# Performance work log

Hardware: AMD Instinct MI355X
Metric: run time of the kernel (lower is better)

## Reference

```python
import jax, jax.numpy as jnp
import numpy as np


def setup_inputs() -> dict:
    key = jax.random.key(0)
    x = jax.random.uniform(key, (64_000_000,), dtype=jnp.float32)
    return {"x": x, "bins": 100}


def reference(x, bins):
    # torch.histc semantics with min=max=0.0: use data min/max as the range.
    xf = x.reshape(-1)
    hmin = jnp.min(xf)
    hmax = jnp.max(xf)
    # guard degenerate range (torch widens it; with random data this is a no-op)
    hmax = jnp.where(hmax == hmin, hmin + 1.0, hmax)
    scale = bins / (hmax - hmin)
    # bin index: floor((x - min) * bins / (max - min)); value == max lands in last bin
    idx = jnp.clip(jnp.floor((xf - hmin) * scale).astype(jnp.int32), 0, bins - 1)
    in_range = (xf >= hmin) & (xf <= hmax)  # out-of-range elements are ignored
    weights = in_range.astype(xf.dtype)
    hist = jax.ops.segment_sum(weights, idx, num_segments=bins)
    return hist
```

## Files before the change

### kernel.cpp

```cpp
#include <hip/hip_runtime.h>

#define NBLOCKS   1024
#define NTHREADS  256
#define UNROLL_A  16
#define UNROLL_B  8
#define NCOPIES   32
#define CSTRIDE   101

__global__ __launch_bounds__(NTHREADS, 4)
void minmax_partial(const float4* __restrict__ x4, long n4,
                    const float* __restrict__ xtail, long ntail,
                    float* __restrict__ pmin, float* __restrict__ pmax,
                    float* __restrict__ out, int bins) {
    __shared__ float smin[NTHREADS / 64], smax[NTHREADS / 64];
    if (blockIdx.x == 0) {
        for (int b = threadIdx.x; b < bins; b += blockDim.x) out[b] = 0.0f;
    }
    const long tid = blockIdx.x * (long)blockDim.x + threadIdx.x;
    const long nth = (long)gridDim.x * blockDim.x;

    float m0 = INFINITY, M0 = -INFINITY, m1 = INFINITY, M1 = -INFINITY;
    float m2 = INFINITY, M2 = -INFINITY, m3 = INFINITY, M3 = -INFINITY;

    const long chunk   = nth * UNROLL_A;
    const long nchunks = n4 / chunk;

    for (long j = nchunks * chunk + tid; j < n4; j += nth) {
        float4 v = x4[j];
        m0 = fminf(m0, fminf(fminf(v.x, v.y), fminf(v.z, v.w)));
        M0 = fmaxf(M0, fmaxf(fmaxf(v.x, v.y), fmaxf(v.z, v.w)));
    }
    for (long j = tid; j < ntail; j += nth) {
        float v = xtail[j];
        m0 = fminf(m0, v);
        M0 = fmaxf(M0, v);
    }
    for (long c = nchunks; c-- > 0;) {
        const long j = c * chunk + tid;
        float4 v[UNROLL_A];
        #pragma unroll
        for (int u = 0; u < UNROLL_A; ++u) v[u] = x4[j + (long)u * nth];
        #pragma unroll
        for (int u = 0; u < UNROLL_A; u += 4) {
            m0 = fminf(m0, fminf(fminf(v[u].x, v[u].y), fminf(v[u].z, v[u].w)));
            M0 = fmaxf(M0, fmaxf(fmaxf(v[u].x, v[u].y), fmaxf(v[u].z, v[u].w)));
            m1 = fminf(m1, fminf(fminf(v[u+1].x, v[u+1].y), fminf(v[u+1].z, v[u+1].w)));
            M1 = fmaxf(M1, fmaxf(fmaxf(v[u+1].x, v[u+1].y), fmaxf(v[u+1].z, v[u+1].w)));
            m2 = fminf(m2, fminf(fminf(v[u+2].x, v[u+2].y), fminf(v[u+2].z, v[u+2].w)));
            M2 = fmaxf(M2, fmaxf(fmaxf(v[u+2].x, v[u+2].y), fmaxf(v[u+2].z, v[u+2].w)));
            m3 = fminf(m3, fminf(fminf(v[u+3].x, v[u+3].y), fminf(v[u+3].z, v[u+3].w)));
            M3 = fmaxf(M3, fmaxf(fmaxf(v[u+3].x, v[u+3].y), fmaxf(v[u+3].z, v[u+3].w)));
        }
    }

    float lm = fminf(fminf(m0, m1), fminf(m2, m3));
    float lM = fmaxf(fmaxf(M0, M1), fmaxf(M2, M3));
    for (int off = 32; off; off >>= 1) {
        lm = fminf(lm, __shfl_xor(lm, off));
        lM = fmaxf(lM, __shfl_xor(lM, off));
    }
    if ((threadIdx.x & 63) == 0) {
        smin[threadIdx.x >> 6] = lm;
        smax[threadIdx.x >> 6] = lM;
    }
    __syncthreads();
    if (threadIdx.x == 0) {
        float bm = smin[0], bM = smax[0];
        for (int w = 1; w < NTHREADS / 64; ++w) { bm = fminf(bm, smin[w]); bM = fmaxf(bM, smax[w]); }
        pmin[blockIdx.x] = bm;
        pmax[blockIdx.x] = bM;
    }
}

__global__ __launch_bounds__(NTHREADS, 4)
void hist_kernel(const float4* __restrict__ x4, long n4,
                 const float* __restrict__ xtail, long ntail,
                 const float* __restrict__ pmin, const float* __restrict__ pmax,
                 float* __restrict__ out, int bins) {
    __shared__ unsigned sh[NCOPIES * CSTRIDE];
    __shared__ float smin[NTHREADS / 64], smax[NTHREADS / 64];
    __shared__ float srange[2];

    float rm = INFINITY, rM = -INFINITY;
    for (int i = threadIdx.x; i < NBLOCKS; i += blockDim.x) {
        rm = fminf(rm, pmin[i]);
        rM = fmaxf(rM, pmax[i]);
    }
    for (int off = 32; off; off >>= 1) {
        rm = fminf(rm, __shfl_xor(rm, off));
        rM = fmaxf(rM, __shfl_xor(rM, off));
    }
    if ((threadIdx.x & 63) == 0) {
        smin[threadIdx.x >> 6] = rm;
        smax[threadIdx.x >> 6] = rM;
    }
    __syncthreads();
    if (threadIdx.x == 0) {
        float bm = smin[0], bM = smax[0];
        for (int w = 1; w < NTHREADS / 64; ++w) { bm = fminf(bm, smin[w]); bM = fmaxf(bM, smax[w]); }
        if (bM == bm) bM = bm + 1.0f;
        srange[0] = bm;
        srange[1] = (float)bins / (bM - bm);
    }
    for (int b = threadIdx.x; b < NCOPIES * CSTRIDE; b += blockDim.x) sh[b] = 0u;
    __syncthreads();

    const float hmin  = srange[0];
    const float scale = srange[1];
    const int   bmax  = bins - 1;
    unsigned* h = sh + (threadIdx.x >> 3) * CSTRIDE;

    const long tid = blockIdx.x * (long)blockDim.x + threadIdx.x;
    const long nth = (long)gridDim.x * blockDim.x;
    const long chunk   = nth * UNROLL_B;
    const long nchunks = n4 / chunk;

    for (long c = 0; c < nchunks; ++c) {
        const long j = c * chunk + tid;
        float4 v[UNROLL_B];
        #pragma unroll
        for (int u = 0; u < UNROLL_B; ++u) v[u] = x4[j + (long)u * nth];
        #pragma unroll
        for (int u = 0; u < UNROLL_B; ++u) {
            int b0 = min(max((int)((v[u].x - hmin) * scale), 0), bmax);
            int b1 = min(max((int)((v[u].y - hmin) * scale), 0), bmax);
            int b2 = min(max((int)((v[u].z - hmin) * scale), 0), bmax);
            int b3 = min(max((int)((v[u].w - hmin) * scale), 0), bmax);
            atomicAdd(&h[b0], 1u);
            atomicAdd(&h[b1], 1u);
            atomicAdd(&h[b2], 1u);
            atomicAdd(&h[b3], 1u);
        }
    }
    for (long j = nchunks * chunk + tid; j < n4; j += nth) {
        float4 v = x4[j];
        int b0 = min(max((int)((v.x - hmin) * scale), 0), bmax);
        int b1 = min(max((int)((v.y - hmin) * scale), 0), bmax);
        int b2 = min(max((int)((v.z - hmin) * scale), 0), bmax);
        int b3 = min(max((int)((v.w - hmin) * scale), 0), bmax);
        atomicAdd(&h[b0], 1u);
        atomicAdd(&h[b1], 1u);
        atomicAdd(&h[b2], 1u);
        atomicAdd(&h[b3], 1u);
    }
    for (long j = tid; j < ntail; j += nth) {
        int b0 = min(max((int)((xtail[j] - hmin) * scale), 0), bmax);
        atomicAdd(&h[b0], 1u);
    }
    __syncthreads();

    for (int b = threadIdx.x; b < bins; b += blockDim.x) {
        unsigned t = 0;
        #pragma unroll
        for (int w = 0; w < NCOPIES; ++w) t += sh[w * CSTRIDE + b];
        if (t) atomicAdd(&out[b], (float)t);
    }
}

extern "C" void kernel_launch(void* const* d_in, const int* in_sizes, int n_in,
                              void* d_out, int out_size, void* d_ws, size_t ws_size,
                              hipStream_t stream) {
    const float* x = (const float*)d_in[0];
    long n = (long)in_sizes[0];
    int bins = out_size;

    long n4 = n >> 2;
    long ntail = n - (n4 << 2);
    const float4* x4 = (const float4*)x;
    const float* xtail = x + (n4 << 2);

    float* out = (float*)d_out;
    float* ws = (float*)d_ws;
    float* pmin = ws;
    float* pmax = ws + NBLOCKS;

    minmax_partial<<<NBLOCKS, NTHREADS, 0, stream>>>(x4, n4, xtail, ntail,
                                                     pmin, pmax, out, bins);
    hist_kernel<<<NBLOCKS, NTHREADS, 0, stream>>>(x4, n4, xtail, ntail,
                                                  pmin, pmax, out, bins);
}
```

Before: 398.5 us.

## Use per-wave contiguous segments and per-lane LDS histogram copies

Both kernels now give each wavefront a contiguous segment of 64*UNROLL float4s in a grid-stride loop over segments, instead of a thread-strided chunked layout. The min/max pass walks segments in reverse order so the histogram pass, which walks them forward, may hit data still in cache. The histogram now keeps 64 LDS copies, one per lane, with stride 101 to cut atomic contention and bank conflicts, and the lower clamp at zero is dropped. The extra copies double LDS use and may lower occupancy. Removing the zero clamp assumes every value is at least the computed minimum.

```diff
diff --git a/kernel.cpp b/kernel.cpp
--- a/kernel.cpp
+++ b/kernel.cpp
@@ -2,9 +2,10 @@
 
 #define NBLOCKS   1024
 #define NTHREADS  256
+#define WPB       (NTHREADS / 64)
 #define UNROLL_A  16
 #define UNROLL_B  8
-#define NCOPIES   32
+#define NCOPIES   64
 #define CSTRIDE   101
 
 __global__ __launch_bounds__(NTHREADS, 4)
@@ -12,34 +13,39 @@
                     const float* __restrict__ xtail, long ntail,
                     float* __restrict__ pmin, float* __restrict__ pmax,
                     float* __restrict__ out, int bins) {
-    __shared__ float smin[NTHREADS / 64], smax[NTHREADS / 64];
+    __shared__ float smin[WPB], smax[WPB];
     if (blockIdx.x == 0) {
         for (int b = threadIdx.x; b < bins; b += blockDim.x) out[b] = 0.0f;
     }
-    const long tid = blockIdx.x * (long)blockDim.x + threadIdx.x;
-    const long nth = (long)gridDim.x * blockDim.x;
+    const int  lane   = threadIdx.x & 63;
+    const long gwave  = blockIdx.x * (long)WPB + (threadIdx.x >> 6);
+    const long nwaves = (long)gridDim.x * WPB;
+    const long SEG    = 64 * UNROLL_A;
+    const long nseg   = n4 / SEG;
 
     float m0 = INFINITY, M0 = -INFINITY, m1 = INFINITY, M1 = -INFINITY;
     float m2 = INFINITY, M2 = -INFINITY, m3 = INFINITY, M3 = -INFINITY;
 
-    const long chunk   = nth * UNROLL_A;
-    const long nchunks = n4 / chunk;
+    {
+        const long tid = blockIdx.x * (long)blockDim.x + threadIdx.x;
+        const long nth = (long)gridDim.x * blockDim.x;
+        for (long j = nseg * SEG + tid; j < n4; j += nth) {
+            float4 v = x4[j];
+            m0 = fminf(m0, fminf(fminf(v.x, v.y), fminf(v.z, v.w)));
+            M0 = fmaxf(M0, fmaxf(fmaxf(v.x, v.y), fmaxf(v.z, v.w)));
+        }
+        for (long j = tid; j < ntail; j += nth) {
+            float v = xtail[j];
+            m0 = fminf(m0, v);
+            M0 = fmaxf(M0, v);
+        }
+    }
 
-    for (long j = nchunks * chunk + tid; j < n4; j += nth) {
-        float4 v = x4[j];
-        m0 = fminf(m0, fminf(fminf(v.x, v.y), fminf(v.z, v.w)));
-        M0 = fmaxf(M0, fmaxf(fmaxf(v.x, v.y), fmaxf(v.z, v.w)));
-    }
-    for (long j = tid; j < ntail; j += nth) {
-        float v = xtail[j];
-        m0 = fminf(m0, v);
-        M0 = fmaxf(M0, v);
-    }
-    for (long c = nchunks; c-- > 0;) {
-        const long j = c * chunk + tid;
+    for (long s = nseg - 1 - gwave; s >= 0; s -= nwaves) {
+        const float4* p = x4 + s * SEG + lane;
         float4 v[UNROLL_A];
         #pragma unroll
-        for (int u = 0; u < UNROLL_A; ++u) v[u] = x4[j + (long)u * nth];
+        for (int u = 0; u < UNROLL_A; ++u) v[u] = p[u * 64];
         #pragma unroll
         for (int u = 0; u < UNROLL_A; u += 4) {
             m0 = fminf(m0, fminf(fminf(v[u].x, v[u].y), fminf(v[u].z, v[u].w)));
@@ -59,14 +65,14 @@
         lm = fminf(lm, __shfl_xor(lm, off));
         lM = fmaxf(lM, __shfl_xor(lM, off));
     }
-    if ((threadIdx.x & 63) == 0) {
+    if (lane == 0) {
         smin[threadIdx.x >> 6] = lm;
         smax[threadIdx.x >> 6] = lM;
     }
     __syncthreads();
     if (threadIdx.x == 0) {
         float bm = smin[0], bM = smax[0];
-        for (int w = 1; w < NTHREADS / 64; ++w) { bm = fminf(bm, smin[w]); bM = fmaxf(bM, smax[w]); }
+        for (int w = 1; w < WPB; ++w) { bm = fminf(bm, smin[w]); bM = fmaxf(bM, smax[w]); }
         pmin[blockIdx.x] = bm;
         pmax[blockIdx.x] = bM;
     }
@@ -78,7 +84,7 @@
                  const float* __restrict__ pmin, const float* __restrict__ pmax,
                  float* __restrict__ out, int bins) {
     __shared__ unsigned sh[NCOPIES * CSTRIDE];
-    __shared__ float smin[NTHREADS / 64], smax[NTHREADS / 64];
+    __shared__ float smin[WPB], smax[WPB];
     __shared__ float srange[2];
 
     float rm = INFINITY, rM = -INFINITY;
@@ -97,7 +103,7 @@
     __syncthreads();
     if (threadIdx.x == 0) {
         float bm = smin[0], bM = smax[0];
-        for (int w = 1; w < NTHREADS / 64; ++w) { bm = fminf(bm, smin[w]); bM = fmaxf(bM, smax[w]); }
+        for (int w = 1; w < WPB; ++w) { bm = fminf(bm, smin[w]); bM = fmaxf(bM, smax[w]); }
         if (bM == bm) bM = bm + 1.0f;
         srange[0] = bm;
         srange[1] = (float)bins / (bM - bm);
@@ -108,51 +114,56 @@
     const float hmin  = srange[0];
     const float scale = srange[1];
     const int   bmax  = bins - 1;
-    unsigned* h = sh + (threadIdx.x >> 3) * CSTRIDE;
+    const int   lane  = threadIdx.x & 63;
+    unsigned* h = sh + lane * CSTRIDE;
 
-    const long tid = blockIdx.x * (long)blockDim.x + threadIdx.x;
-    const long nth = (long)gridDim.x * blockDim.x;
-    const long chunk   = nth * UNROLL_B;
-    const long nchunks = n4 / chunk;
+    const long gwave  = blockIdx.x * (long)WPB + (threadIdx.x >> 6);
+    const long nwaves = (long)gridDim.x * WPB;
+    const long SEG    = 64 * UNROLL_B;
+    const long nseg   = n4 / SEG;
 
-    for (long c = 0; c < nchunks; ++c) {
-        const long j = c * chunk + tid;
+    for (long s = gwave; s < nseg; s += nwaves) {
+        const float4* p = x4 + s * SEG + lane;
         float4 v[UNROLL_B];
         #pragma unroll
-        for (int u = 0; u < UNROLL_B; ++u) v[u] = x4[j + (long)u * nth];
+        for (int u = 0; u < UNROLL_B; ++u) v[u] = p[u * 64];
         #pragma unroll
         for (int u = 0; u < UNROLL_B; ++u) {
-            int b0 = min(max((int)((v[u].x - hmin) * scale), 0), bmax);
-            int b1 = min(max((int)((v[u].y - hmin) * scale), 0), bmax);
-            int b2 = min(max((int)((v[u].z - hmin) * scale), 0), bmax);
-            int b3 = min(max((int)((v[u].w - hmin) * scale), 0), bmax);
+            int b0 = min((int)((v[u].x - hmin) * scale), bmax);
+            int b1 = min((int)((v[u].y - hmin) * scale), bmax);
+            int b2 = min((int)((v[u].z - hmin) * scale), bmax);
+            int b3 = min((int)((v[u].w - hmin) * scale), bmax);
             atomicAdd(&h[b0], 1u);
             atomicAdd(&h[b1], 1u);
             atomicAdd(&h[b2], 1u);
             atomicAdd(&h[b3], 1u);
         }
     }
-    for (long j = nchunks * chunk + tid; j < n4; j += nth) {
-        float4 v = x4[j];
-        int b0 = min(max((int)((v.x - hmin) * scale), 0), bmax);
-        int b1 = min(max((int)((v.y - hmin) * scale), 0), bmax);
-        int b2 = min(max((int)((v.z - hmin) * scale), 0), bmax);
-        int b3 = min(max((int)((v.w - hmin) * scale), 0), bmax);
-        atomicAdd(&h[b0], 1u);
-        atomicAdd(&h[b1], 1u);
-        atomicAdd(&h[b2], 1u);
-        atomicAdd(&h[b3], 1u);
-    }
-    for (long j = tid; j < ntail; j += nth) {
-        int b0 = min(max((int)((xtail[j] - hmin) * scale), 0), bmax);
-        atomicAdd(&h[b0], 1u);
+    {
+        const long tid = blockIdx.x * (long)blockDim.x + threadIdx.x;
+        const long nth = (long)gridDim.x * blockDim.x;
+        for (long j = nseg * SEG + tid; j < n4; j += nth) {
+            float4 v = x4[j];
+            int b0 = min((int)((v.x - hmin) * scale), bmax);
+            int b1 = min((int)((v.y - hmin) * scale), bmax);
+            int b2 = min((int)((v.z - hmin) * scale), bmax);
+            int b3 = min((int)((v.w - hmin) * scale), bmax);
+            atomicAdd(&h[b0], 1u);
+            atomicAdd(&h[b1], 1u);
+            atomicAdd(&h[b2], 1u);
+            atomicAdd(&h[b3], 1u);
+        }
+        for (long j = tid; j < ntail; j += nth) {
+            int b0 = min((int)((xtail[j] - hmin) * scale), bmax);
+            atomicAdd(&h[b0], 1u);
+        }
     }
     __syncthreads();
 
     for (int b = threadIdx.x; b < bins; b += blockDim.x) {
         unsigned t = 0;
-        #pragma unroll
-        for (int w = 0; w < NCOPIES; ++w) t += sh[w * CSTRIDE + b];
+        #pragma unroll 8
+        for (int c = 0; c < NCOPIES; ++c) t += sh[c * CSTRIDE + b];
         if (t) atomicAdd(&out[b], (float)t);
     }
 }
```

Measured after the change: 398.4 us. About the same (-0.0%).
